# Optimization experiments

Measured on AMD Instinct MI355X. Metric: run time of the kernel, lower is better.

## Reference

```python
import jax, jax.numpy as jnp
import numpy as np

EPS = 1e-5
TEMP = 50.0


def setup_inputs() -> dict:
    key = jax.random.key(0)
    features = jax.random.normal(key, (4, 64, 128, 128), dtype=jnp.float32)
    return {"features": features, "patch_sim_neiref_neisimavgsize": 5}


def reference(features, patch_sim_neiref_neisimavgsize):
    k = patch_sim_neiref_neisimavgsize
    B, C, H, W = features.shape
    pad = k // 2
    xp = jnp.pad(features, ((0, 0), (0, 0), (pad, pad), (pad, pad)))
    # windows ordered (kh, kw) to match F.unfold: [B, k*k, C, H, W]
    wins = jnp.stack([xp[:, :, i:i + H, j:j + W]
                      for i in range(k) for j in range(k)], axis=1)
    # [B, H, W, k*k, C]
    patch = jnp.transpose(wins, (0, 3, 4, 1, 2)) + EPS
    patch_norm = patch / jnp.sqrt(jnp.sum(patch * patch, axis=-1, keepdims=True))
    center = patch_norm[..., (k * k) // 2:(k * k) // 2 + 1, :]  # center pixel of window
    sim = jnp.sum(patch_norm * center, axis=-1, keepdims=True)   # cosine sim [B,H,W,kk,1]
    wei = jax.nn.softmax(TEMP * sim, axis=-2)
    repr_vec = jnp.sum(patch * wei, axis=-2)                     # [B,H,W,C]
    return jnp.transpose(repr_vec, (0, 3, 1, 2))                 # [B,C,H,W]
```

## Files before the change

kernel.cpp:

```cpp
#include <hip/hip_runtime.h>

#define EPS 1e-5f
#define TEMP 50.0f
#define CCH 64
#define HH 128
#define WW 128
#define HWSZ (HH * WW)
#define CEPS2 (CCH * EPS * EPS)

#define ITW 8
#define ITH 4
#define HTW 12
#define HTH 8
#define HPX (HTW * HTH)
#define HPAD 97

typedef _Float16 h16;
typedef h16 h2v __attribute__((ext_vector_type(2)));
typedef h16 h8v __attribute__((ext_vector_type(8)));
union H8 { h8v v; h2v p[4]; };

__device__ __forceinline__ float fdot2(h2v a, h2v b, float c) {
#if __has_builtin(__builtin_amdgcn_fdot2)
    return __builtin_amdgcn_fdot2(a, b, c, false);
#else
    return c + (float)a[0] * (float)b[0] + (float)a[1] * (float)b[1];
#endif
}

__device__ __forceinline__ float quad_sum(float x) {
#if __has_builtin(__builtin_amdgcn_mov_dpp)
    int i = __builtin_bit_cast(int, x);
    int a = __builtin_amdgcn_mov_dpp(i, 0xB1, 0xF, 0xF, true);
    float x1 = x + __builtin_bit_cast(float, a);
    int j = __builtin_bit_cast(int, x1);
    int b = __builtin_amdgcn_mov_dpp(j, 0x4E, 0xF, 0xF, true);
    return x1 + __builtin_bit_cast(float, b);
#else
    float x1 = x + __shfl_xor(x, 1);
    return x1 + __shfl_xor(x1, 2);
#endif
}

#define TP_PAD 72
__global__ __launch_bounds__(256) void rv_transpose(const float* __restrict__ x,
                                                    h16* __restrict__ xt) {
    __shared__ h16 buf[WW][TP_PAD];
    const int t = threadIdx.x;
    const int h = blockIdx.x;
    const int b = blockIdx.y;
    const float* src = x + (size_t)b * (CCH * HWSZ) + h * WW;
#pragma unroll 8
    for (int i = 0; i < 32; ++i) {
        int k = i * 256 + t;
        int c = k >> 7;
        int w = k & 127;
        buf[w][c] = (h16)src[(size_t)c * HWSZ + w];
    }
    __syncthreads();
    h16* dst = xt + (size_t)(b * HH + h) * WW * CCH;
#pragma unroll
    for (int j = 0; j < 4; ++j) {
        int idx = j * 256 + t;
        int w = idx >> 3;
        int q = idx & 7;
        h8v v = *(const h8v*)&buf[w][q * 8];
        *(h8v*)&dst[(size_t)w * CCH + q * 8] = v;
    }
}

__global__ __launch_bounds__(128, 4) void rv_fused(const h16* __restrict__ xt,
                                                   float* __restrict__ out) {
    __shared__ h8v  tile[8][HPAD];
    __shared__ float sh_q[HPX];

    const int t  = threadIdx.x;
    const int w0 = blockIdx.x * ITW;
    const int h0 = blockIdx.y * ITH;
    const int b  = blockIdx.z;

#pragma unroll
    for (int it = 0; it < 6; ++it) {
        int k = it * 128 + t;
        int q  = k & 7;
        int px = k >> 3;
        int row = px / HTW;
        int col = px - row * HTW;
        int gh = h0 + row - 2;
        int gw = w0 + col - 2;
        h8v v = {};
        if (gh >= 0 && gh < HH && gw >= 0 && gw < WW) {
            v = *(const h8v*)&xt[((size_t)(b * HH + gh) * WW + gw) * CCH + q * 8];
        }
        tile[q][px] = v;
    }
    __syncthreads();

    if (t < HPX) {
        float q = 0.f;
#pragma unroll
        for (int hq = 0; hq < 8; ++hq) {
            H8 u; u.v = tile[hq][t];
#pragma unroll
            for (int j = 0; j < 4; ++j) q = fdot2(u.p[j], u.p[j], q);
        }
        sh_q[t] = q;
    }
    __syncthreads();

    const int qg  = t & 3;
    const int pix = t >> 2;
    const int r   = pix >> 3;
    const int cl  = pix & 7;
    const int cpx = (r + 2) * HTW + (cl + 2);

    const float rinvC = rsqrtf(sh_q[cpx] + CEPS2);

    H8 ctr0, ctr1;
    ctr0.v = tile[2 * qg][cpx];
    ctr1.v = tile[2 * qg + 1][cpx];

    h2v acc[8] = {};
    float wsum = 0.f;

#pragma unroll
    for (int dr = 0; dr < 5; ++dr) {
#pragma unroll
        for (int dc = 0; dc < 5; ++dc) {
            const int npx = (r + dr) * HTW + (cl + dc);
            H8 a0, a1;
            a0.v = tile[2 * qg][npx];
            a1.v = tile[2 * qg + 1][npx];
            float d = 0.f;
#pragma unroll
            for (int j = 0; j < 4; ++j) d = fdot2(ctr0.p[j], a0.p[j], d);
#pragma unroll
            for (int j = 0; j < 4; ++j) d = fdot2(ctr1.p[j], a1.p[j], d);
            d = quad_sum(d);
            const float N2n = sh_q[npx] + CEPS2;
            const float sim = (d + CEPS2) * (rsqrtf(N2n) * rinvC);
            const float wn = __expf(fmaf(TEMP, sim, -TEMP));
            wsum += wn;
            const h16 wh = (h16)wn;
            const h2v w2 = {wh, wh};
#pragma unroll
            for (int j = 0; j < 4; ++j) {
                acc[j]     = a0.p[j] * w2 + acc[j];
                acc[4 + j] = a1.p[j] * w2 + acc[4 + j];
            }
        }
    }

    const float rs = 1.f / wsum;
    const size_t obase = (size_t)b * (CCH * HWSZ)
                       + (size_t)(qg * 16) * HWSZ
                       + (h0 + r) * WW + (w0 + cl);
#pragma unroll
    for (int j = 0; j < 8; ++j) {
        const float f0 = (float)acc[j][0];
        const float f1 = (float)acc[j][1];
        out[obase + (size_t)(2 * j) * HWSZ]     = fmaf(f0, rs, EPS);
        out[obase + (size_t)(2 * j + 1) * HWSZ] = fmaf(f1, rs, EPS);
    }
}

extern "C" void kernel_launch(void* const* d_in, const int* in_sizes, int n_in,
                              void* d_out, int out_size, void* d_ws, size_t ws_size,
                              hipStream_t stream) {
    const float* x = (const float*)d_in[0];
    float* outp = (float*)d_out;
    h16* xt = (h16*)d_ws;

    rv_transpose<<<dim3(HH, 4), dim3(256), 0, stream>>>(x, xt);
    rv_fused<<<dim3(WW / ITW, HH / ITH, 4), dim3(128, 1, 1), 0, stream>>>(xt, outp);
}
```

Before: 82.73 us.

## Fuse NCHW-to-channel-last transpose into main kernel's halo tile load

```diff
diff --git a/kernel.cpp b/kernel.cpp
--- a/kernel.cpp
+++ b/kernel.cpp
@@ -42,35 +42,8 @@
 #endif
 }
 
-#define TP_PAD 72
-__global__ __launch_bounds__(256) void rv_transpose(const float* __restrict__ x,
-                                                    h16* __restrict__ xt) {
-    __shared__ h16 buf[WW][TP_PAD];
-    const int t = threadIdx.x;
-    const int h = blockIdx.x;
-    const int b = blockIdx.y;
-    const float* src = x + (size_t)b * (CCH * HWSZ) + h * WW;
-#pragma unroll 8
-    for (int i = 0; i < 32; ++i) {
-        int k = i * 256 + t;
-        int c = k >> 7;
-        int w = k & 127;
-        buf[w][c] = (h16)src[(size_t)c * HWSZ + w];
-    }
-    __syncthreads();
-    h16* dst = xt + (size_t)(b * HH + h) * WW * CCH;
-#pragma unroll
-    for (int j = 0; j < 4; ++j) {
-        int idx = j * 256 + t;
-        int w = idx >> 3;
-        int q = idx & 7;
-        h8v v = *(const h8v*)&buf[w][q * 8];
-        *(h8v*)&dst[(size_t)w * CCH + q * 8] = v;
-    }
-}
-
-__global__ __launch_bounds__(128, 4) void rv_fused(const h16* __restrict__ xt,
-                                                   float* __restrict__ out) {
+__global__ __launch_bounds__(128, 4) void rv_one(const float* __restrict__ x,
+                                                 float* __restrict__ out) {
     __shared__ h8v  tile[8][HPAD];
     __shared__ float sh_q[HPX];
 
@@ -78,21 +51,28 @@
     const int w0 = blockIdx.x * ITW;
     const int h0 = blockIdx.y * ITH;
     const int b  = blockIdx.z;
+    const float* xb = x + (size_t)b * (CCH * HWSZ);
 
+    const int c   = t & 63;
+    const int q8  = c >> 3;
+    const int sub = c & 7;
+    const float* cp = xb + (size_t)c * HWSZ;
 #pragma unroll
-    for (int it = 0; it < 6; ++it) {
-        int k = it * 128 + t;
-        int q  = k & 7;
-        int px = k >> 3;
-        int row = px / HTW;
-        int col = px - row * HTW;
-        int gh = h0 + row - 2;
-        int gw = w0 + col - 2;
-        h8v v = {};
-        if (gh >= 0 && gh < HH && gw >= 0 && gw < WW) {
-            v = *(const h8v*)&xt[((size_t)(b * HH + gh) * WW + gw) * CCH + q * 8];
+    for (int i = 0; i < 4; ++i) {
+        const int row = (t >> 6) + 2 * i;
+        const int gh = h0 + row - 2;
+        const bool rowok = (unsigned)gh < (unsigned)HH;
+        const float* rp = cp + gh * WW + (w0 - 2);
+        h16* dst = (h16*)&tile[q8][row * HTW];
+#pragma unroll
+        for (int k = 0; k < 6; ++k) {
+            const int gw = w0 - 2 + 2 * k;
+            float2 v = make_float2(0.f, 0.f);
+            if (rowok && (unsigned)gw < (unsigned)WW)
+                v = *(const float2*)(rp + 2 * k);
+            dst[(2 * k) * 8 + sub]     = (h16)v.x;
+            dst[(2 * k + 1) * 8 + sub] = (h16)v.y;
         }
-        tile[q][px] = v;
     }
     __syncthreads();
 
@@ -169,8 +149,5 @@
                               hipStream_t stream) {
     const float* x = (const float*)d_in[0];
     float* outp = (float*)d_out;
-    h16* xt = (h16*)d_ws;
-
-    rv_transpose<<<dim3(HH, 4), dim3(256), 0, stream>>>(x, xt);
-    rv_fused<<<dim3(WW / ITW, HH / ITH, 4), dim3(128, 1, 1), 0, stream>>>(xt, outp);
+    rv_one<<<dim3(WW / ITW, HH / ITH, 4), dim3(128, 1, 1), 0, stream>>>(x, outp);
 }
```

Measured after the change: 133.1 us. +60.9%, slower.
